# Kernel tuning notes

Measured on AMD Instinct MI355X. Metric: run time of the kernel, lower is better.

Reference implementation:

```python
import jax, jax.numpy as jnp
import numpy as np

T, N, E = 6, 50000, 1600000
NFEAT, NHID, NCLASS = 256, 256, 16
SLOPE = 11.0 / 48.0  # eval-mode RReLU: mean of default (lower=1/8, upper=1/3)


def _grcu(H_seq, src, dst, val, Wz, Uz, bz, Wr, Ur, br, Wh, Uh, bh, Q0):
    """One GRCU layer: matrix-GRU weight evolution + sparse GCN aggregation per step.
    H_seq: [T, N, in]  src/dst: [T, E] int  val: [T, E]  Q0: [in, out]."""
    n = H_seq.shape[1]

    def step(Q, xs):
        H, s, d, v = xs
        # mat_GRU_cell: x = hidden = prev_Q (z_topk path is unused in this repo's forward)
        z = jax.nn.sigmoid(Wz @ Q + Uz @ Q + bz)
        r = jax.nn.sigmoid(Wr @ Q + Ur @ Q + br)
        h = jnp.tanh(Wh @ Q + Uh @ (r * Q) + bh)
        Qn = (1.0 - z) * Q + z * h
        XW = H @ Qn                                   # [N, out]
        msg = v[:, None] * XW[s]                      # per-edge gather: Ahat row weights
        agg = jax.ops.segment_sum(msg, d, num_segments=n)  # Ahat @ (H @ Qn)
        out = jnp.where(agg >= 0, agg, SLOPE * agg)   # RReLU (eval)
        return Qn, out

    _, out_seq = jax.lax.scan(step, Q0, (H_seq, src, dst, val))
    return out_seq  # [T, N, out]


def setup_inputs() -> dict:
    key = jax.random.key(0)
    ks = iter(jax.random.split(key, 64))

    def rn(shape, scale=0.05):
        return jax.random.normal(next(ks), shape, dtype=jnp.float32) * scale

    inp = {
        "node_feats": jax.random.normal(next(ks), (T, N, NFEAT), dtype=jnp.float32),
        "edge_val": jax.random.uniform(next(ks), (T, E), dtype=jnp.float32),
    }
    for l, (fi, fo) in enumerate([(NFEAT, NHID), (NHID, NHID)]):
        for g in ("z", "r", "h"):
            inp[f"l{l}_W{g}"] = rn((fi, fi))
            inp[f"l{l}_U{g}"] = rn((fi, fi))
            inp[f"l{l}_b{g}"] = jnp.zeros((fi, fo), dtype=jnp.float32)
        inp[f"l{l}_Q0"] = rn((fi, fo))
    inp["mlp_W1"] = rn((NHID, NHID))
    inp["mlp_b1"] = jnp.zeros((NHID,), dtype=jnp.float32)
    inp["mlp_W2"] = rn((NHID, NCLASS))
    inp["mlp_b2"] = jnp.zeros((NCLASS,), dtype=jnp.float32)
    inp["edge_src"] = jax.random.randint(next(ks), (T, E), 0, N, dtype=jnp.int32)
    inp["edge_dst"] = jax.random.randint(next(ks), (T, E), 0, N, dtype=jnp.int32)
    return inp


def reference(node_feats, edge_val,
              l0_Wz, l0_Uz, l0_bz, l0_Wr, l0_Ur, l0_br, l0_Wh, l0_Uh, l0_bh, l0_Q0,
              l1_Wz, l1_Uz, l1_bz, l1_Wr, l1_Ur, l1_br, l1_Wh, l1_Uh, l1_bh, l1_Q0,
              mlp_W1, mlp_b1, mlp_W2, mlp_b2,
              edge_src, edge_dst):
    h1 = _grcu(node_feats, edge_src, edge_dst, edge_val,
               l0_Wz, l0_Uz, l0_bz, l0_Wr, l0_Ur, l0_br, l0_Wh, l0_Uh, l0_bh, l0_Q0)
    h2 = _grcu(h1, edge_src, edge_dst, edge_val,
               l1_Wz, l1_Uz, l1_bz, l1_Wr, l1_Ur, l1_br, l1_Wh, l1_Uh, l1_bh, l1_Q0)
    out = h2[-1]                                    # last timestep, [N, nhid]
    hid = jax.nn.relu(out @ mlp_W1 + mlp_b1)
    logits = hid @ mlp_W2 + mlp_b2
    return jax.nn.log_softmax(logits, axis=1)       # [N, nclass]
```

## Files before the change

### kernel.cpp

```cpp
#include <hip/hip_runtime.h>
#include <cstddef>

#define SLOPE_F (11.0f / 48.0f)

static const int NN = 50000;
static const int EE = 1600000;
static const int D  = 256;
static const int NCH = 196;
static const int GB  = 391;

typedef __attribute__((ext_vector_type(8))) short short8;
typedef __attribute__((ext_vector_type(4))) float f32x4;
typedef __attribute__((ext_vector_type(2))) float f32x2;

__device__ __forceinline__ ushort f2bf(float f) {
    unsigned u = __float_as_uint(f);
    unsigned r = (u + 0x7fffu + ((u >> 16) & 1u)) >> 16;
    return (ushort)r;
}
__device__ __forceinline__ float bf2f(ushort u) {
    return __uint_as_float(((unsigned)u) << 16);
}

__device__ __forceinline__ unsigned char enc8(float x) {
    unsigned ux = __float_as_uint(x);
    unsigned sign = (ux >> 31) << 7;
    float ax = __uint_as_float(ux & 0x7fffffffu);
    if (!(ax < 448.f)) return (unsigned char)(sign | 0x7E);
    if (ax < 0.015625f) {
        int m = (int)(ax * 512.f + 0.5f);
        if (m > 7) return (unsigned char)(sign | 0x08);
        return (unsigned char)(sign | m);
    }
    unsigned u = __float_as_uint(ax);
    u += 0x7FFFFu + ((u >> 20) & 1u);
    int e = (int)((u >> 23) & 255) - 127 + 7;
    if (e > 15) return (unsigned char)(sign | 0x7E);
    return (unsigned char)(sign | (e << 3) | ((u >> 20) & 7));
}

__global__ __launch_bounds__(256) void prephist_kernel(
        const float* __restrict__ Wz0, const float* __restrict__ Uz0,
        const float* __restrict__ Wr0, const float* __restrict__ Ur0,
        const float* __restrict__ Wh0, const float* __restrict__ Uh0,
        const float* __restrict__ Wz1, const float* __restrict__ Uz1,
        const float* __restrict__ Wr1, const float* __restrict__ Ur1,
        const float* __restrict__ Wh1, const float* __restrict__ Uh1,
        const float* __restrict__ W1,
        ushort* __restrict__ WB, ushort* __restrict__ BtW1,
        const int* __restrict__ dst, int* __restrict__ deg) {
    int b = blockIdx.x;
    int tid = threadIdx.x;
    if (b >= 144) {
        int e = (b - 144) * 256 + tid;
        if (e < EE) atomicAdd(&deg[dst[e]], 1);
        return;
    }
    __shared__ float lt[64][65];
    if (b < 128) {
        int mat = b >> 4;
        int tr = (b >> 2) & 3, tc = b & 3;
        const float* P = nullptr; const float* S = nullptr;
        switch (mat) {
            case 0: P = Wz0; S = Uz0; break;
            case 1: P = Wr0; S = Ur0; break;
            case 2: P = Wh0; break;
            case 3: P = Uh0; break;
            case 4: P = Wz1; S = Uz1; break;
            case 5: P = Wr1; S = Ur1; break;
            case 6: P = Wh1; break;
            default: P = Uh1; break;
        }
#pragma unroll
        for (int r0 = 0; r0 < 64; r0 += 4) {
            int r = r0 + (tid >> 6);
            int c = tid & 63;
            int row = tr * 64 + r, col = tc * 64 + c;
            float v = P[row * 256 + col];
            if (S) v += S[row * 256 + col];
            lt[r][c] = v;
        }
        __syncthreads();
#pragma unroll
        for (int c0 = 0; c0 < 64; c0 += 4) {
            int c = c0 + (tid >> 6);
            int r = tid & 63;
            WB[(size_t)mat * 65536 + (size_t)(tc * 64 + c) * 256 + tr * 64 + r] =
                f2bf(lt[r][c]);
        }
    } else {
        int t = b - 128;
        int tr = (t >> 2) & 3, tc = t & 3;
#pragma unroll
        for (int r0 = 0; r0 < 64; r0 += 4) {
            int r = r0 + (tid >> 6);
            int c = tid & 63;
            lt[r][c] = W1[(tr * 64 + r) * 256 + tc * 64 + c];
        }
        __syncthreads();
#pragma unroll
        for (int c0 = 0; c0 < 64; c0 += 4) {
            int c = c0 + (tid >> 6);
            int r = tid & 63;
            BtW1[(size_t)(tc * 64 + c) * 256 + tr * 64 + r] = f2bf(lt[r][c]);
        }
    }
}

__global__ __launch_bounds__(256) void gruscan_kernel(
        const ushort* __restrict__ WB,
        const float* __restrict__ bz0, const float* __restrict__ br0,
        const float* __restrict__ bh0, const float* __restrict__ Q00,
        const float* __restrict__ bz1, const float* __restrict__ br1,
        const float* __restrict__ bh1, const float* __restrict__ Q01,
        ushort* __restrict__ Bt,
        const int* __restrict__ deg, int* __restrict__ rs, int* __restrict__ cur,
        int* __restrict__ bsum, int* __restrict__ boff, int* __restrict__ done) {
    int tid = threadIdx.x;
    if (blockIdx.x >= 512) {
        __shared__ int wsum[4];
        __shared__ int lastflag;
        int blk = blockIdx.x - 512;
        int i = blk * 256 + tid;
        int lane = tid & 63, wv = tid >> 6;
        int v = (i < NN) ? deg[i] : 0;
        int x = v;
#pragma unroll
        for (int off = 1; off < 64; off <<= 1) {
            int t = __shfl_up(x, off, 64);
            if (lane >= off) x += t;
        }
        if (lane == 63) wsum[wv] = x;
        __syncthreads();
        if (tid == 0) {
            int s = 0;
#pragma unroll
            for (int q = 0; q < 4; ++q) { int t = wsum[q]; wsum[q] = s; s += t; }
            bsum[blk] = s;
        }
        __syncthreads();
        if (i < NN) { int p = wsum[wv] + x - v; rs[i] = p; cur[i] = p; }
        __threadfence();
        if (tid == 0) lastflag = (atomicAdd(done, 1) == NCH - 1);
        __syncthreads();
        if (lastflag) {
            __threadfence();
            int bv = (tid < NCH) ? bsum[tid] : 0;
            int bx = bv;
#pragma unroll
            for (int off = 1; off < 64; off <<= 1) {
                int t = __shfl_up(bx, off, 64);
                if (lane >= off) bx += t;
            }
            if (lane == 63) wsum[wv] = bx;
            __syncthreads();
            if (tid == 0) {
                int s = 0;
#pragma unroll
                for (int q = 0; q < 4; ++q) { int t = wsum[q]; wsum[q] = s; s += t; }
            }
            __syncthreads();
            if (tid < NCH) boff[tid] = wsum[wv] + bx - bv;
        }
        return;
    }
    __shared__ float qs[256];
    __shared__ float rqs[256];
    int layer = blockIdx.x >> 8;
    int j = blockIdx.x & 255;
    int i = tid;
    const ushort* Mz = WB + ((size_t)layer * 4 + 0) * 65536;
    const ushort* Mr = WB + ((size_t)layer * 4 + 1) * 65536;
    const ushort* Wh = WB + ((size_t)layer * 4 + 2) * 65536;
    const ushort* Uh = WB + ((size_t)layer * 4 + 3) * 65536;
    const float* bz = layer ? bz1 : bz0;
    const float* br = layer ? br1 : br0;
    const float* bh = layer ? bh1 : bh0;
    const float* Q0 = layer ? Q01 : Q00;

    float bzv = bz[i * 256 + j];
    float brv = br[i * 256 + j];
    float bhv = bh[i * 256 + j];

    qs[i] = Q0[i * 256 + j];
    __syncthreads();

    for (int step = 0; step < 6; ++step) {
        float az = 0.f, ar = 0.f, ah = 0.f;
#pragma unroll 8
        for (int k = 0; k < 256; ++k) {
            float q = qs[k];
            az += bf2f(Mz[k * 256 + i]) * q;
            ar += bf2f(Mr[k * 256 + i]) * q;
            ah += bf2f(Wh[k * 256 + i]) * q;
        }
        float zz = 1.f / (1.f + expf(-(az + bzv)));
        float rr = 1.f / (1.f + expf(-(ar + brv)));
        float qo = qs[i];
        rqs[i] = rr * qo;
        __syncthreads();
        float bu = 0.f;
#pragma unroll 8
        for (int k = 0; k < 256; ++k)
            bu += bf2f(Uh[k * 256 + i]) * rqs[k];
        float h = tanhf(ah + bu + bhv);
        float qn = (1.f - zz) * qo + zz * h;
        __syncthreads();
        qs[i] = qn;
        __syncthreads();
    }
    Bt[(size_t)layer * 65536 + (size_t)j * 256 + i] = f2bf(qs[i]);
}

template <int ASRC, int EPI>
__device__ __forceinline__ void gemm_body(int bid, int tid,
                                          const ushort* __restrict__ A,
                                          const float* __restrict__ Af,
                                          const ushort* __restrict__ Bt,
                                          const float* __restrict__ bias,
                                          unsigned char* __restrict__ C8,
                                          ushort* __restrict__ Cb, int M) {
    int w = tid >> 6, l = tid & 63;
    int lr = l & 15;
    int lk = l >> 4;
    int row0 = bid * 128 + w * 32;
    int ra = row0 + lr;      if (ra > M - 1) ra = M - 1;
    int rb = row0 + 16 + lr; if (rb > M - 1) rb = M - 1;
    const ushort* Ap0  = A  + (size_t)ra * 256 + lk * 8;
    const ushort* Ap1  = A  + (size_t)rb * 256 + lk * 8;
    const float*  Apf0 = Af + (size_t)ra * 256 + lk * 8;
    const float*  Apf1 = Af + (size_t)rb * 256 + lk * 8;
    const ushort* Bp   = Bt + (size_t)lr * 256 + lk * 8;

    f32x4 acc0[16] = {};
    f32x4 acc1[16] = {};
#pragma unroll
    for (int kc = 0; kc < 8; ++kc) {
        short8 a0, a1;
        if (ASRC == 0) {
            a0 = *(const short8*)(Ap0 + kc * 32);
            a1 = *(const short8*)(Ap1 + kc * 32);
        } else {
            float4 f0 = *(const float4*)(Apf0 + kc * 32);
            float4 f1 = *(const float4*)(Apf0 + kc * 32 + 4);
            float4 g0 = *(const float4*)(Apf1 + kc * 32);
            float4 g1 = *(const float4*)(Apf1 + kc * 32 + 4);
            a0[0] = (short)f2bf(f0.x); a0[1] = (short)f2bf(f0.y);
            a0[2] = (short)f2bf(f0.z); a0[3] = (short)f2bf(f0.w);
            a0[4] = (short)f2bf(f1.x); a0[5] = (short)f2bf(f1.y);
            a0[6] = (short)f2bf(f1.z); a0[7] = (short)f2bf(f1.w);
            a1[0] = (short)f2bf(g0.x); a1[1] = (short)f2bf(g0.y);
            a1[2] = (short)f2bf(g0.z); a1[3] = (short)f2bf(g0.w);
            a1[4] = (short)f2bf(g1.x); a1[5] = (short)f2bf(g1.y);
            a1[6] = (short)f2bf(g1.z); a1[7] = (short)f2bf(g1.w);
        }
#pragma unroll
        for (int nb = 0; nb < 16; ++nb) {
            short8 bf = *(const short8*)(Bp + (size_t)nb * 4096 + kc * 32);
            acc0[nb] = __builtin_amdgcn_mfma_f32_16x16x32_bf16(a0, bf, acc0[nb], 0, 0, 0);
            acc1[nb] = __builtin_amdgcn_mfma_f32_16x16x32_bf16(a1, bf, acc1[nb], 0, 0, 0);
        }
    }

    int ro = lk * 4;
#pragma unroll
    for (int nb = 0; nb < 16; ++nb) {
        int gc = nb * 16 + lr;
        float bb = (EPI == 1) ? bias[gc] : 0.f;
#pragma unroll
        for (int q = 0; q < 4; ++q) {
            int g0 = row0 + ro + q;
            if (g0 < M) {
                float v = acc0[nb][q];
                if (EPI == 1) {
                    Cb[(size_t)g0 * 256 + gc] = f2bf(fmaxf(v + bb, 0.f));
                } else {
                    C8[(size_t)g0 * 256 + gc] = enc8(v);
                }
            }
            int g1 = row0 + 16 + ro + q;
            if (g1 < M) {
                float v = acc1[nb][q];
                if (EPI == 1) {
                    Cb[(size_t)g1 * 256 + gc] = f2bf(fmaxf(v + bb, 0.f));
                } else {
                    C8[(size_t)g1 * 256 + gc] = enc8(v);
                }
            }
        }
    }
}

template <int ASRC, int EPI>
__global__ __launch_bounds__(256) void gemm_mfma(const ushort* __restrict__ A,
                                                 const float* __restrict__ Af,
                                                 const ushort* __restrict__ Bt,
                                                 const float* __restrict__ bias,
                                                 unsigned char* __restrict__ C8,
                                                 ushort* __restrict__ Cb, int M) {
    gemm_body<ASRC, EPI>(blockIdx.x, threadIdx.x, A, Af, Bt, bias, C8, Cb, M);
}

__global__ __launch_bounds__(256) void gemsca_kernel(const float* __restrict__ Af,
                                                     const ushort* __restrict__ Bt,
                                                     unsigned char* __restrict__ C8, int M,
                                                     const int* __restrict__ src,
                                                     const int* __restrict__ dst,
                                                     const float* __restrict__ val,
                                                     int* __restrict__ cur,
                                                     const int* __restrict__ boff,
                                                     unsigned long long* __restrict__ csr) {
    if (blockIdx.x < GB) {
        gemm_body<1, 0>(blockIdx.x, threadIdx.x, nullptr, Af, Bt, nullptr, C8, nullptr, M);
        return;
    }
    int e = (blockIdx.x - GB) * 256 + threadIdx.x;
    if (e < EE) {
        int d = dst[e];
        int p = atomicAdd(&cur[d], 1) + boff[d >> 8];
        unsigned long long pk = (unsigned long long)(unsigned)src[e]
                              | ((unsigned long long)(unsigned)__float_as_uint(val[e]) << 32);
        __builtin_nontemporal_store(pk, &csr[p]);
    }
}

__global__ __launch_bounds__(256) void agg_csr_kernel(const unsigned char* __restrict__ XW,
                                                      const int2* __restrict__ csr,
                                                      const int* __restrict__ rs,
                                                      const int* __restrict__ boff,
                                                      ushort* __restrict__ out) {
    int d = blockIdx.x * 4 + (threadIdx.x >> 6);
    if (d >= NN) return;
    int l = threadIdx.x & 63;
    int h = l >> 5;
    int il = l & 31;
    int beg = rs[d] + boff[d >> 8];
    int end = (d + 1 < NN) ? (rs[d + 1] + boff[(d + 1) >> 8]) : EE;
    float a0 = 0.f, a1 = 0.f, a2 = 0.f, a3 = 0.f;
    float a4 = 0.f, a5 = 0.f, a6 = 0.f, a7 = 0.f;
    int i = beg + h;
    for (; i + 14 < end; i += 16) {
        int2 e[8];
        uint2 x[8];
#pragma unroll
        for (int u = 0; u < 8; ++u) e[u] = csr[i + 2 * u];
#pragma unroll
        for (int u = 0; u < 8; ++u)
            x[u] = *(const uint2*)&XW[(size_t)e[u].x * 256 + il * 8];
#pragma unroll
        for (int u = 0; u < 8; ++u) {
            float v = __int_as_float(e[u].y);
            f32x2 p0 = __builtin_amdgcn_cvt_pk_f32_fp8(x[u].x, false);
            f32x2 p1 = __builtin_amdgcn_cvt_pk_f32_fp8(x[u].x, true);
            f32x2 p2 = __builtin_amdgcn_cvt_pk_f32_fp8(x[u].y, false);
            f32x2 p3 = __builtin_amdgcn_cvt_pk_f32_fp8(x[u].y, true);
            a0 += v * p0.x; a1 += v * p0.y; a2 += v * p1.x; a3 += v * p1.y;
            a4 += v * p2.x; a5 += v * p2.y; a6 += v * p3.x; a7 += v * p3.y;
        }
    }
    for (; i < end; i += 2) {
        int2 e0 = csr[i];
        float v = __int_as_float(e0.y);
        uint2 x0 = *(const uint2*)&XW[(size_t)e0.x * 256 + il * 8];
        f32x2 p0 = __builtin_amdgcn_cvt_pk_f32_fp8(x0.x, false);
        f32x2 p1 = __builtin_amdgcn_cvt_pk_f32_fp8(x0.x, true);
        f32x2 p2 = __builtin_amdgcn_cvt_pk_f32_fp8(x0.y, false);
        f32x2 p3 = __builtin_amdgcn_cvt_pk_f32_fp8(x0.y, true);
        a0 += v * p0.x; a1 += v * p0.y; a2 += v * p1.x; a3 += v * p1.y;
        a4 += v * p2.x; a5 += v * p2.y; a6 += v * p3.x; a7 += v * p3.y;
    }
    a0 += __shfl_xor(a0, 32); a1 += __shfl_xor(a1, 32);
    a2 += __shfl_xor(a2, 32); a3 += __shfl_xor(a3, 32);
    a4 += __shfl_xor(a4, 32); a5 += __shfl_xor(a5, 32);
    a6 += __shfl_xor(a6, 32); a7 += __shfl_xor(a7, 32);
    if (h == 0) {
        float r[8] = {a0, a1, a2, a3, a4, a5, a6, a7};
        short8 o;
#pragma unroll
        for (int c = 0; c < 8; ++c) {
            float v = r[c];
            v = (v >= 0.f) ? v : SLOPE_F * v;
            o[c] = (short)f2bf(v);
        }
        *(short8*)&out[(size_t)d * D + il * 8] = o;
    }
}

__global__ void mlp2_kernel(const ushort* __restrict__ hid, const float* __restrict__ W2,
                            const float* __restrict__ b2, float* __restrict__ out, int M) {
    int tid = threadIdx.x;
    int n = blockIdx.x * 16 + (tid >> 4);
    int c = tid & 15;
    if (n >= M) return;
    float acc = b2[c];
    const ushort* hp = hid + (size_t)n * D;
    for (int k = 0; k < D; k += 8) {
        short8 h8 = *(const short8*)(hp + k);
#pragma unroll
        for (int u = 0; u < 8; ++u)
            acc += bf2f((ushort)h8[u]) * W2[(k + u) * 16 + c];
    }
    float m = acc;
#pragma unroll
    for (int off = 1; off < 16; off <<= 1)
        m = fmaxf(m, __shfl_xor(m, off, 16));
    float ex = expf(acc - m);
    float s = ex;
#pragma unroll
    for (int off = 1; off < 16; off <<= 1)
        s += __shfl_xor(s, off, 16);
    out[(size_t)n * 16 + c] = acc - m - logf(s);
}

extern "C" void kernel_launch(void* const* d_in, const int* in_sizes, int n_in,
                              void* d_out, int out_size, void* d_ws, size_t ws_size,
                              hipStream_t stream) {
    const float* node_feats = (const float*)d_in[0];
    const float* edge_val   = (const float*)d_in[1];
    const float* l0_Wz = (const float*)d_in[2];
    const float* l0_Uz = (const float*)d_in[3];
    const float* l0_bz = (const float*)d_in[4];
    const float* l0_Wr = (const float*)d_in[5];
    const float* l0_Ur = (const float*)d_in[6];
    const float* l0_br = (const float*)d_in[7];
    const float* l0_Wh = (const float*)d_in[8];
    const float* l0_Uh = (const float*)d_in[9];
    const float* l0_bh = (const float*)d_in[10];
    const float* l0_Q0 = (const float*)d_in[11];
    const float* l1_Wz = (const float*)d_in[12];
    const float* l1_Uz = (const float*)d_in[13];
    const float* l1_bz = (const float*)d_in[14];
    const float* l1_Wr = (const float*)d_in[15];
    const float* l1_Ur = (const float*)d_in[16];
    const float* l1_br = (const float*)d_in[17];
    const float* l1_Wh = (const float*)d_in[18];
    const float* l1_Uh = (const float*)d_in[19];
    const float* l1_bh = (const float*)d_in[20];
    const float* l1_Q0 = (const float*)d_in[21];
    const float* W1 = (const float*)d_in[22];
    const float* b1 = (const float*)d_in[23];
    const float* W2 = (const float*)d_in[24];
    const float* b2 = (const float*)d_in[25];
    const int* e_src = (const int*)d_in[26];
    const int* e_dst = (const int*)d_in[27];
    float* out = (float*)d_out;

    const size_t BIG = (size_t)NN * D;
    unsigned char* XW8 = (unsigned char*)d_ws;
    ushort* H   = (ushort*)(XW8 + BIG);
    ushort* HID = H + BIG;
    ushort* Bt  = HID + BIG;
    ushort* WB  = Bt + 3 * 65536;
    int2*   csr = (int2*)(WB + 8 * 65536);
    int*    deg = (int*)(csr + EE);
    int*    done = deg + NN;
    int*    rs  = done + 1;
    int*    cur = rs + NN;
    int*    bsum = cur + NN;
    int*    boff = bsum + 200;

    const float* feats5 = node_feats + (size_t)5 * BIG;
    const int*   src5   = e_src + (size_t)5 * EE;
    const int*   dst5   = e_dst + (size_t)5 * EE;
    const float* val5   = edge_val + (size_t)5 * EE;

    hipMemsetAsync(deg, 0, (NN + 1) * sizeof(int), stream);

    const int histblocks = (EE + 255) / 256;
    prephist_kernel<<<144 + histblocks, 256, 0, stream>>>(
        l0_Wz, l0_Uz, l0_Wr, l0_Ur, l0_Wh, l0_Uh,
        l1_Wz, l1_Uz, l1_Wr, l1_Ur, l1_Wh, l1_Uh,
        W1, WB, Bt + 2 * 65536, dst5, deg);

    gruscan_kernel<<<512 + NCH, 256, 0, stream>>>(WB, l0_bz, l0_br, l0_bh, l0_Q0,
                                                  l1_bz, l1_br, l1_bh, l1_Q0, Bt,
                                                  deg, rs, cur, bsum, boff, done);

    gemsca_kernel<<<GB + histblocks, 256, 0, stream>>>(feats5, Bt + 0 * 65536, XW8, NN,
                                                       src5, dst5, val5, cur, boff,
                                                       (unsigned long long*)csr);

    const int ablocks = (NN + 3) / 4;

    agg_csr_kernel<<<ablocks, 256, 0, stream>>>(XW8, csr, rs, boff, H);

    gemm_mfma<0, 0><<<GB, 256, 0, stream>>>(H, nullptr, Bt + 1 * 65536, nullptr,
                                            XW8, nullptr, NN);
    agg_csr_kernel<<<ablocks, 256, 0, stream>>>(XW8, csr, rs, boff, H);

    gemm_mfma<0, 1><<<GB, 256, 0, stream>>>(H, nullptr, Bt + 2 * 65536, b1,
                                            nullptr, HID, NN);
    mlp2_kernel<<<(NN + 15) / 16, 256, 0, stream>>>(HID, W2, b2, out, NN);
}
```

Measured before the change: 681.0 us.

## Pack fp8 GEMM output into 16-byte stores with permuted column layout

The fp8 epilogue of the GEMM now packs 16 encoded bytes per lane and writes them with one uint4 store, instead of writing one byte at a time. Because each lane holds a strided set of columns, XW is stored in a permuted column order. The SpMM gather stays the same, and the final per-node write undoes the permutation when storing the bf16 output. The cost is that the coalesced short8 output store in the aggregation kernel becomes eight scattered 2-byte stores.

```diff
diff --git a/kernel.cpp b/kernel.cpp
--- a/kernel.cpp
+++ b/kernel.cpp
@@ -22,21 +22,21 @@
     return __uint_as_float(((unsigned)u) << 16);
 }
 
-__device__ __forceinline__ unsigned char enc8(float x) {
+__device__ __forceinline__ unsigned enc8(float x) {
     unsigned ux = __float_as_uint(x);
     unsigned sign = (ux >> 31) << 7;
     float ax = __uint_as_float(ux & 0x7fffffffu);
-    if (!(ax < 448.f)) return (unsigned char)(sign | 0x7E);
+    if (!(ax < 448.f)) return sign | 0x7E;
     if (ax < 0.015625f) {
         int m = (int)(ax * 512.f + 0.5f);
-        if (m > 7) return (unsigned char)(sign | 0x08);
-        return (unsigned char)(sign | m);
+        if (m > 7) return sign | 0x08;
+        return sign | m;
     }
     unsigned u = __float_as_uint(ax);
     u += 0x7FFFFu + ((u >> 20) & 1u);
     int e = (int)((u >> 23) & 255) - 127 + 7;
-    if (e > 15) return (unsigned char)(sign | 0x7E);
-    return (unsigned char)(sign | (e << 3) | ((u >> 20) & 7));
+    if (e > 15) return sign | 0x7E;
+    return sign | (e << 3) | ((u >> 20) & 7);
 }
 
 __global__ __launch_bounds__(256) void prephist_kernel(
@@ -263,29 +263,38 @@
     }
 
     int ro = lk * 4;
-#pragma unroll
-    for (int nb = 0; nb < 16; ++nb) {
-        int gc = nb * 16 + lr;
-        float bb = (EPI == 1) ? bias[gc] : 0.f;
+    if (EPI == 0) {
 #pragma unroll
         for (int q = 0; q < 4; ++q) {
+            unsigned w0[4], w1[4];
+#pragma unroll
+            for (int t = 0; t < 4; ++t) {
+                unsigned x0 = 0, x1 = 0;
+#pragma unroll
+                for (int u = 0; u < 4; ++u) {
+                    x0 |= enc8(acc0[t * 4 + u][q]) << (8 * u);
+                    x1 |= enc8(acc1[t * 4 + u][q]) << (8 * u);
+                }
+                w0[t] = x0; w1[t] = x1;
+            }
             int g0 = row0 + ro + q;
-            if (g0 < M) {
-                float v = acc0[nb][q];
-                if (EPI == 1) {
-                    Cb[(size_t)g0 * 256 + gc] = f2bf(fmaxf(v + bb, 0.f));
-                } else {
-                    C8[(size_t)g0 * 256 + gc] = enc8(v);
-                }
-            }
+            if (g0 < M)
+                *(uint4*)&C8[(size_t)g0 * 256 + lr * 16] = make_uint4(w0[0], w0[1], w0[2], w0[3]);
             int g1 = row0 + 16 + ro + q;
-            if (g1 < M) {
-                float v = acc1[nb][q];
-                if (EPI == 1) {
-                    Cb[(size_t)g1 * 256 + gc] = f2bf(fmaxf(v + bb, 0.f));
-                } else {
-                    C8[(size_t)g1 * 256 + gc] = enc8(v);
-                }
+            if (g1 < M)
+                *(uint4*)&C8[(size_t)g1 * 256 + lr * 16] = make_uint4(w1[0], w1[1], w1[2], w1[3]);
+        }
+    } else {
+#pragma unroll
+        for (int nb = 0; nb < 16; ++nb) {
+            int gc = nb * 16 + lr;
+            float bb = bias[gc];
+#pragma unroll
+            for (int q = 0; q < 4; ++q) {
+                int g0 = row0 + ro + q;
+                if (g0 < M) Cb[(size_t)g0 * 256 + gc] = f2bf(fmaxf(acc0[nb][q] + bb, 0.f));
+                int g1 = row0 + 16 + ro + q;
+                if (g1 < M) Cb[(size_t)g1 * 256 + gc] = f2bf(fmaxf(acc1[nb][q] + bb, 0.f));
             }
         }
     }
@@ -375,14 +384,14 @@
     a6 += __shfl_xor(a6, 32); a7 += __shfl_xor(a7, 32);
     if (h == 0) {
         float r[8] = {a0, a1, a2, a3, a4, a5, a6, a7};
-        short8 o;
-#pragma unroll
-        for (int c = 0; c < 8; ++c) {
-            float v = r[c];
+#pragma unroll
+        for (int u = 0; u < 8; ++u) {
+            int p = il * 8 + u;
+            int c = ((p & 15) << 4) | (p >> 4);
+            float v = r[u];
             v = (v >= 0.f) ? v : SLOPE_F * v;
-            o[c] = (short)f2bf(v);
-        }
-        *(short8*)&out[(size_t)d * D + il * 8] = o;
+            out[(size_t)d * D + c] = f2bf(v);
+        }
     }
 }
 
```

Result: faster. 653.5 us (-4.0%).
